# Kernel optimization log

Measured on AMD Instinct MI355X. Metric: run time of the kernel, lower is better.

## Reference

```python
import jax, jax.numpy as jnp
import numpy as np

N_NODES = 100000
N_EDGES = 1600000
HIDDEN = 64
EPS = 1e-5


def setup_inputs() -> dict:
    key = jax.random.key(0)
    ks = jax.random.split(key, 12)
    h = HIDDEN
    inp = {
        'x': jax.random.normal(ks[0], (N_NODES, h), dtype=jnp.float32),
        'edge_index': jax.random.randint(ks[1], (2, N_EDGES), 0, N_NODES, dtype=jnp.int32),
        'message': jax.random.normal(ks[2], (N_EDGES, h), dtype=jnp.float32),
        # node_mlp: Linear(2h->h), BN(h), ReLU, Dropout(identity), Linear(h->h), BN(h), ReLU
        'W1': jax.random.normal(ks[3], (2 * h, h), dtype=jnp.float32) / np.sqrt(2.0 * h),
        'b1': jnp.zeros((h,), jnp.float32),
        'g1': jnp.ones((h,), jnp.float32),
        'be1': jnp.zeros((h,), jnp.float32),
        'W2': jax.random.normal(ks[4], (h, h), dtype=jnp.float32) / np.sqrt(h),
        'b2': jnp.zeros((h,), jnp.float32),
        'g2': jnp.ones((h,), jnp.float32),
        'be2': jnp.zeros((h,), jnp.float32),
        # attention_mlp: Linear(h->1), Sigmoid
        'Wa': jax.random.normal(ks[5], (h, 1), dtype=jnp.float32) / np.sqrt(h),
        'ba': jnp.zeros((1,), jnp.float32),
    }
    return inp


def _scatter_max(msg, idx, n):
    # torch_scatter scatter(..., reduce='max') fills segments with no edges with 0
    agg = jax.ops.segment_max(msg, idx, num_segments=n)  # [N, H], -inf where empty
    cnt = jax.ops.segment_sum(jnp.ones((idx.shape[0],), msg.dtype), idx, num_segments=n)
    return jnp.where(cnt[:, None] > 0, agg, jnp.zeros((), msg.dtype))


def _batchnorm(x, gamma, beta):
    # training-mode BatchNorm1d: batch mean / biased variance
    mu = jnp.mean(x, axis=0)
    var = jnp.mean((x - mu) ** 2, axis=0)
    return (x - mu) * jax.lax.rsqrt(var + EPS) * gamma + beta


def reference(x, edge_index, message, W1, b1, g1, be1, W2, b2, g2, be2, Wa, ba):
    n = x.shape[0]
    row, col = edge_index[0], edge_index[1]
    fwd = _scatter_max(message, col, n)   # [N, H]
    bwd = _scatter_max(message, row, n)   # [N, H]
    out = jnp.concatenate([fwd, bwd], axis=1)          # [N, 2H]
    h1 = jax.nn.relu(_batchnorm(out @ W1 + b1, g1, be1))  # dropout = identity (eval)
    h2 = jax.nn.relu(_batchnorm(h1 @ W2 + b2, g2, be2))   # [N, H]
    att = jax.nn.sigmoid(h2 @ Wa + ba).reshape(-1)          # [N]
    return (h2, att)
```

## Files before the change

### kernel.cpp

```cpp
#include <hip/hip_runtime.h>
#include <hip/hip_bf16.h>
#include <cstdint>
#include <cstddef>

#define HDIM 64
#define EPS 1e-5f
#define BN 128
#define BSH 7
#define NXCD 8
#define BCAPX 2560
#define CURPAD 16
#define SENTE 128u
static const unsigned SENT = 0x007FFFFFu;

typedef short bf16x8 __attribute__((ext_vector_type(8)));
typedef float f32x4  __attribute__((ext_vector_type(4)));
typedef float f4v    __attribute__((ext_vector_type(4)));
typedef unsigned u2v __attribute__((ext_vector_type(2)));
typedef unsigned u4v __attribute__((ext_vector_type(4)));

__device__ __forceinline__ unsigned bf16rn(float f) {
    unsigned u = __float_as_uint(f);
    return (u + 0x7FFFu + ((u >> 16) & 1u)) >> 16;
}

__device__ __forceinline__ unsigned flipf(float f) {
    unsigned u = __float_as_uint(f);
    return u ^ (((unsigned)((int)u >> 31)) | 0x80000000u);
}

__device__ __forceinline__ float unflip(unsigned u) {
    if (u == SENT) return 0.0f;
    unsigned b = (u & 0x80000000u) ? (u & 0x7FFFFFFFu) : ~u;
    return __uint_as_float(b);
}

__global__ __launch_bounds__(256) void fill_kernel(
    const int* __restrict__ ei, unsigned* __restrict__ bcur,
    unsigned* __restrict__ entries,
    const float* __restrict__ W1, const float* __restrict__ W2,
    unsigned short* __restrict__ W1T, unsigned short* __restrict__ W2T,
    int E, int nblk, int eblocks) {
    int blk = blockIdx.x;
    if (blk >= eblocks) {
        int t = (blk - eblocks) * 256 + threadIdx.x;
        if (t < 128 * 64) {
            int k = t >> 6, o = t & 63;
            W1T[o * 128 + k] = (unsigned short)bf16rn(W1[t]);
        } else {
            int t2 = t - 128 * 64;
            if (t2 < 64 * 64) {
                int k = t2 >> 6, o = t2 & 63;
                W2T[o * 64 + k] = (unsigned short)bf16rn(W2[t2]);
            }
        }
        return;
    }
    int e = blk * 256 + threadIdx.x;
    if (e >= E) return;
    unsigned xcd;
    asm volatile("s_getreg_b32 %0, hwreg(HW_REG_XCC_ID)" : "=s"(xcd));
    xcd &= (NXCD - 1);
    int row = ei[e];
    int col = ei[(size_t)E + e];
    unsigned cell1 = (unsigned)(col >> BSH) * NXCD + xcd;
    unsigned cell2 = (unsigned)(nblk + (row >> BSH)) * NXCD + xcd;
    unsigned p1 = atomicAdd(&bcur[(size_t)cell1 * CURPAD], 1u);
    unsigned p2 = atomicAdd(&bcur[(size_t)cell2 * CURPAD], 1u);
    if (p1 < BCAPX)
        entries[(size_t)cell1 * BCAPX + p1] = ((unsigned)e << 8) | (unsigned)(col & (BN - 1));
    if (p2 < BCAPX)
        entries[(size_t)cell2 * BCAPX + p2] = ((unsigned)e << 8) | (unsigned)(row & (BN - 1));
}

__global__ __launch_bounds__(256) void binned_max_kernel(
    const float* __restrict__ msg, const unsigned* __restrict__ bcur,
    const unsigned* __restrict__ entries,
    unsigned short* __restrict__ fwdB, unsigned short* __restrict__ bwdB,
    int N, int nblk) {
    __shared__ __align__(16) unsigned acc[(BN + 1) * HDIM];
    int tid = threadIdx.x;
    int wave = tid >> 6, lane = tid & 63;
    int b = blockIdx.x;

    {
        u4v sv; sv.x = SENT; sv.y = SENT; sv.z = SENT; sv.w = SENT;
        u4v* p = (u4v*)acc;
        for (int i = tid; i < (BN + 1) * HDIM / 4; i += 256) p[i] = sv;
    }
    __syncthreads();

    unsigned accBase = (unsigned)(size_t)&acc[0];
    unsigned laneOff = accBase + ((unsigned)lane << 2);

    for (int rr = 0; rr < 2; ++rr) {
        int r = wave + rr * 4;
        unsigned cnt = bcur[((size_t)b * NXCD + r) * CURPAD];
        if (cnt > BCAPX) cnt = BCAPX;
        if (cnt == 0) continue;
        const unsigned* rb = entries + ((size_t)b * NXCD + r) * BCAPX;

        unsigned cur = ((unsigned)lane < cnt) ? rb[lane] : SENTE;
        float v[16];
#pragma unroll
        for (int k = 0; k < 16; ++k) {
            unsigned ent = __shfl(cur, k);
            v[k] = __builtin_nontemporal_load(&msg[(size_t)(ent >> 8) * HDIM + lane]);
        }

        for (unsigned c0 = 0; c0 < cnt; c0 += 64) {
            unsigned rem = cnt - c0;
            unsigned nxt = SENTE;
            bool havenxt = (c0 + 64 < cnt);
            if (havenxt)
                nxt = (c0 + 64 + (unsigned)lane < cnt) ? rb[c0 + 64 + lane] : SENTE;
#pragma unroll
            for (int b16 = 0; b16 < 4; ++b16) {
                if ((unsigned)(b16 * 16) >= rem) break;
                bool hn = (c0 + (unsigned)((b16 + 1) * 16) < cnt);
                float vn[16];
                if (hn) {
                    unsigned src = (b16 < 3) ? cur : nxt;
                    int kb = (b16 < 3) ? (b16 + 1) * 16 : 0;
#pragma unroll
                    for (int k = 0; k < 16; ++k) {
                        unsigned ent = __shfl(src, kb + k);
                        vn[k] = __builtin_nontemporal_load(
                            &msg[(size_t)(ent >> 8) * HDIM + lane]);
                    }
                }
#pragma unroll
                for (int k = 0; k < 16; ++k) {
                    unsigned ent = __shfl(cur, b16 * 16 + k);
                    unsigned addr = laneOff + ((ent & 255u) << 8);
                    asm volatile("ds_max_u32 %0, %1" :: "v"(addr), "v"(flipf(v[k])));
                }
                if (hn) {
#pragma unroll
                    for (int k = 0; k < 16; ++k) v[k] = vn[k];
                }
            }
            cur = nxt;
        }
    }
    asm volatile("" ::: "memory");
    __syncthreads();

    bool fwd = (b < nblk);
    int node0 = (fwd ? b : b - nblk) * BN;
    unsigned short* dst = fwd ? fwdB : bwdB;
    for (int i = tid; i < BN * (HDIM / 4); i += 256) {
        int rrow = i >> 4, c4 = (i & 15) * 4;
        int node = node0 + rrow;
        if (node >= N) continue;
        uint4 a = *(const uint4*)&acc[rrow * HDIM + c4];
        float v0 = unflip(a.x), v1 = unflip(a.y);
        float v2 = unflip(a.z), v3 = unflip(a.w);
        u2v o;
        o.x = bf16rn(v0) | (bf16rn(v1) << 16);
        o.y = bf16rn(v2) | (bf16rn(v3) << 16);
        *(u2v*)(dst + (size_t)node * HDIM + c4) = o;
    }
}


__global__ __launch_bounds__(256) void gemm1_mfma_kernel(
    const unsigned short* __restrict__ fwdB, const unsigned short* __restrict__ bwdB,
    const unsigned short* __restrict__ W1T, const float* __restrict__ b1,
    float* __restrict__ y1, float* __restrict__ sum1, float* __restrict__ sq1, int N) {
    __shared__ float wsum[4][64], wsq[4][64];
    int tid = threadIdx.x;
    int wave = tid >> 6, lane = tid & 63;
    int lrow = lane & 15, kseg = lane >> 4;
    int rbase = blockIdx.x * 64 + wave * 16;

    bf16x8 bfr[4][4];
#pragma unroll
    for (int nt = 0; nt < 4; ++nt)
#pragma unroll
        for (int kb = 0; kb < 4; ++kb)
            bfr[nt][kb] = *(const bf16x8*)(W1T + (size_t)(nt * 16 + lrow) * 128 + kb * 32 + kseg * 8);

    int r = rbase + lrow;
    bool ok = (r < N);
    size_t ro = (size_t)(ok ? r : 0) * HDIM;
    bf16x8 z = {};
    bf16x8 afr[4];
    afr[0] = *(const bf16x8*)(fwdB + ro + kseg * 8);
    afr[1] = *(const bf16x8*)(fwdB + ro + 32 + kseg * 8);
    afr[2] = *(const bf16x8*)(bwdB + ro + kseg * 8);
    afr[3] = *(const bf16x8*)(bwdB + ro + 32 + kseg * 8);
    if (!ok) { afr[0] = z; afr[1] = z; afr[2] = z; afr[3] = z; }

    f32x4 acc[4] = {};
#pragma unroll
    for (int kb = 0; kb < 4; ++kb)
#pragma unroll
        for (int nt = 0; nt < 4; ++nt)
            acc[nt] = __builtin_amdgcn_mfma_f32_16x16x32_bf16(afr[kb], bfr[nt][kb], acc[nt], 0, 0, 0);

#pragma unroll
    for (int nt = 0; nt < 4; ++nt) {
        int col = nt * 16 + lrow;
        float bias = b1[col];
        float s = 0.f, q = 0.f;
#pragma unroll
        for (int rr = 0; rr < 4; ++rr) {
            int rowi = rbase + kseg * 4 + rr;
            if (rowi < N) {
                float v = acc[nt][rr] + bias;
                y1[(size_t)rowi * HDIM + col] = v;
                s += v; q += v * v;
            }
        }
        s += __shfl_xor(s, 16); s += __shfl_xor(s, 32);
        q += __shfl_xor(q, 16); q += __shfl_xor(q, 32);
        if (kseg == 0) { wsum[wave][col] = s; wsq[wave][col] = q; }
    }
    __syncthreads();
    if (tid < 64) {
        float S = wsum[0][tid] + wsum[1][tid] + wsum[2][tid] + wsum[3][tid];
        float Q = wsq[0][tid] + wsq[1][tid] + wsq[2][tid] + wsq[3][tid];
        atomicAdd(&sum1[tid], S);
        atomicAdd(&sq1[tid], Q);
    }
}

__global__ __launch_bounds__(256) void gemm2_mfma_kernel(
    const float* __restrict__ y1, const float* __restrict__ sum1, const float* __restrict__ sq1,
    const float* __restrict__ g1, const float* __restrict__ be1,
    const unsigned short* __restrict__ W2T, const float* __restrict__ b2,
    float* __restrict__ y2, float* __restrict__ sum2, float* __restrict__ sq2, int N) {
    __shared__ float sc[64], sh[64];
    __shared__ float wsum[4][64], wsq[4][64];
    int tid = threadIdx.x;
    if (tid < 64) {
        float invN = 1.0f / (float)N;
        float mu = sum1[tid] * invN;
        float var = sq1[tid] * invN - mu * mu;
        float rs = rsqrtf(var + EPS);
        float s = rs * g1[tid];
        sc[tid] = s;
        sh[tid] = be1[tid] - mu * s;
    }
    __syncthreads();
    int wave = tid >> 6, lane = tid & 63;
    int lrow = lane & 15, kseg = lane >> 4;
    int rbase = blockIdx.x * 64 + wave * 16;

    bf16x8 bfr[4][2];
#pragma unroll
    for (int nt = 0; nt < 4; ++nt)
#pragma unroll
        for (int kb = 0; kb < 2; ++kb)
            bfr[nt][kb] = *(const bf16x8*)(W2T + (size_t)(nt * 16 + lrow) * 64 + kb * 32 + kseg * 8);

    int r = rbase + lrow;
    size_t ro = (size_t)((r < N) ? r : 0) * HDIM;
    bf16x8 afr[2];
#pragma unroll
    for (int kb = 0; kb < 2; ++kb) {
        const f4v* yp = (const f4v*)(y1 + ro + kb * 32 + kseg * 8);
        f4v u0 = yp[0], u1 = yp[1];
        int k0 = kb * 32 + kseg * 8;
        bf16x8 a;
#pragma unroll
        for (int j = 0; j < 4; ++j) {
            float h0 = fmaxf(fmaf(u0[j], sc[k0 + j], sh[k0 + j]), 0.f);
            float h1 = fmaxf(fmaf(u1[j], sc[k0 + 4 + j], sh[k0 + 4 + j]), 0.f);
            a[j] = (short)bf16rn(h0);
            a[4 + j] = (short)bf16rn(h1);
        }
        afr[kb] = a;
    }

    f32x4 acc[4] = {};
#pragma unroll
    for (int kb = 0; kb < 2; ++kb)
#pragma unroll
        for (int nt = 0; nt < 4; ++nt)
            acc[nt] = __builtin_amdgcn_mfma_f32_16x16x32_bf16(afr[kb], bfr[nt][kb], acc[nt], 0, 0, 0);

#pragma unroll
    for (int nt = 0; nt < 4; ++nt) {
        int col = nt * 16 + lrow;
        float bias = b2[col];
        float s = 0.f, q = 0.f;
#pragma unroll
        for (int rr = 0; rr < 4; ++rr) {
            int rowi = rbase + kseg * 4 + rr;
            if (rowi < N) {
                float v = acc[nt][rr] + bias;
                y2[(size_t)rowi * HDIM + col] = v;
                s += v; q += v * v;
            }
        }
        s += __shfl_xor(s, 16); s += __shfl_xor(s, 32);
        q += __shfl_xor(q, 16); q += __shfl_xor(q, 32);
        if (kseg == 0) { wsum[wave][col] = s; wsq[wave][col] = q; }
    }
    __syncthreads();
    if (tid < 64) {
        float S = wsum[0][tid] + wsum[1][tid] + wsum[2][tid] + wsum[3][tid];
        float Q = wsq[0][tid] + wsq[1][tid] + wsq[2][tid] + wsq[3][tid];
        atomicAdd(&sum2[tid], S);
        atomicAdd(&sq2[tid], Q);
    }
}

__global__ __launch_bounds__(256) void final_kernel(
    const float* __restrict__ y2, const float* __restrict__ sum2, const float* __restrict__ sq2,
    const float* __restrict__ g2, const float* __restrict__ be2,
    const float* __restrict__ Wa, const float* __restrict__ ba,
    float* __restrict__ out_h2, float* __restrict__ out_att, int N) {
    __shared__ float sc[HDIM], sh[HDIM], wa[HDIM];
    __shared__ float bav;
    if (threadIdx.x < HDIM) {
        int c = threadIdx.x;
        float invN = 1.0f / (float)N;
        float mu = sum2[c] * invN;
        float var = sq2[c] * invN - mu * mu;
        float rstd = rsqrtf(var + EPS);
        float s = rstd * g2[c];
        sc[c] = s;
        sh[c] = be2[c] - mu * s;
        wa[c] = Wa[c];
    }
    if (threadIdx.x == 0) bav = ba[0];
    __syncthreads();
    int n = blockIdx.x * 256 + threadIdx.x;
    if (n >= N) return;

    const f4v* p = (const f4v*)&y2[(size_t)n * HDIM];
    f4v* dst = (f4v*)&out_h2[(size_t)n * HDIM];
    float att = bav;
#pragma unroll 1
    for (int kk = 0; kk < 16; ++kk) {
        f4v u = p[kk];
        f4v hv;
#pragma unroll
        for (int j = 0; j < 4; ++j) {
            int k = kk * 4 + j;
            float h = fmaxf(fmaf(u[j], sc[k], sh[k]), 0.0f);
            hv[j] = h;
            att = fmaf(h, wa[k], att);
        }
        dst[kk] = hv;
    }
    out_att[n] = 1.0f / (1.0f + expf(-att));
}

extern "C" void kernel_launch(void* const* d_in, const int* in_sizes, int n_in,
                              void* d_out, int out_size, void* d_ws, size_t ws_size,
                              hipStream_t stream) {
    const int*   ei   = (const int*)d_in[1];
    const float* msg  = (const float*)d_in[2];
    const float* W1   = (const float*)d_in[3];
    const float* b1   = (const float*)d_in[4];
    const float* g1   = (const float*)d_in[5];
    const float* be1  = (const float*)d_in[6];
    const float* W2   = (const float*)d_in[7];
    const float* b2   = (const float*)d_in[8];
    const float* g2   = (const float*)d_in[9];
    const float* be2  = (const float*)d_in[10];
    const float* Wa   = (const float*)d_in[11];
    const float* ba   = (const float*)d_in[12];

    const int N = in_sizes[0] / HDIM;
    const int E = in_sizes[1] / 2;
    const int nblk = (N + BN - 1) / BN;

    unsigned short* fwdB = (unsigned short*)d_ws;
    unsigned short* bwdB = fwdB + (size_t)N * HDIM;
    unsigned short* W1T  = bwdB + (size_t)N * HDIM;
    unsigned short* W2T  = W1T + 8192;
    float*    stats      = (float*)(W2T + 4096);
    unsigned* bcur       = (unsigned*)(stats + 256);
    unsigned* entries    = bcur + (size_t)2 * nblk * NXCD * CURPAD;
    float*    y1         = (float*)d_out;
    float*    y2         = (float*)d_ws;
    float*    out_att    = (float*)d_out + (size_t)N * HDIM;

    hipMemsetAsync(stats, 0, 256 * sizeof(float)
                             + (size_t)2 * nblk * NXCD * CURPAD * sizeof(unsigned), stream);

    int eblocks = (E + 255) / 256;
    fill_kernel<<<eblocks + 48, 256, 0, stream>>>(ei, bcur, entries, W1, W2,
                                                  W1T, W2T, E, nblk, eblocks);

    binned_max_kernel<<<2 * nblk, 256, 0, stream>>>(msg, bcur, entries, fwdB, bwdB, N, nblk);

    int G = (N + 63) / 64;
    gemm1_mfma_kernel<<<G, 256, 0, stream>>>(fwdB, bwdB, W1T, b1, y1,
                                             stats, stats + 64, N);
    gemm2_mfma_kernel<<<G, 256, 0, stream>>>(y1, stats, stats + 64, g1, be1,
                                             W2T, b2, y2, stats + 128, stats + 192, N);
    final_kernel<<<(N + 255) / 256, 256, 0, stream>>>(y2, stats + 128, stats + 192,
                                                      g2, be2, Wa, ba,
                                                      (float*)d_out, out_att, N);
}
```

Measured before the change: 439.3 us.

## Use 16-byte vector message loads with padded LDS rows in binned max

Each lane in the binned max kernel now loads four contiguous floats with a 16-byte nontemporal load, so one wave instruction covers four edges at a time instead of one. To limit bank conflicts when four edges from the same wave hit different rows, the LDS accumulator rows are padded to a stride of 68 words. The old software prefetch of the next batch of messages is removed, which cuts register pressure but may expose more load latency.

Result: faster. 428.9 us, median of 2 (-2.4%).

```diff
diff --git a/kernel.cpp b/kernel.cpp
--- a/kernel.cpp
+++ b/kernel.cpp
@@ -11,6 +11,7 @@
 #define BCAPX 2560
 #define CURPAD 16
 #define SENTE 128u
+#define LSTRIDE 68
 static const unsigned SENT = 0x007FFFFFu;
 
 typedef short bf16x8 __attribute__((ext_vector_type(8)));
@@ -78,20 +79,21 @@
     const unsigned* __restrict__ entries,
     unsigned short* __restrict__ fwdB, unsigned short* __restrict__ bwdB,
     int N, int nblk) {
-    __shared__ __align__(16) unsigned acc[(BN + 1) * HDIM];
+    __shared__ __align__(16) unsigned acc[(BN + 1) * LSTRIDE];
     int tid = threadIdx.x;
     int wave = tid >> 6, lane = tid & 63;
+    int part = lane & 15, grp = lane >> 4;
     int b = blockIdx.x;
 
     {
         u4v sv; sv.x = SENT; sv.y = SENT; sv.z = SENT; sv.w = SENT;
         u4v* p = (u4v*)acc;
-        for (int i = tid; i < (BN + 1) * HDIM / 4; i += 256) p[i] = sv;
+        for (int i = tid; i < (BN + 1) * LSTRIDE / 4; i += 256) p[i] = sv;
     }
     __syncthreads();
 
     unsigned accBase = (unsigned)(size_t)&acc[0];
-    unsigned laneOff = accBase + ((unsigned)lane << 2);
+    unsigned partOff = accBase + ((unsigned)part << 4);
 
     for (int rr = 0; rr < 2; ++rr) {
         int r = wave + rr * 4;
@@ -100,47 +102,30 @@
         if (cnt == 0) continue;
         const unsigned* rb = entries + ((size_t)b * NXCD + r) * BCAPX;
 
-        unsigned cur = ((unsigned)lane < cnt) ? rb[lane] : SENTE;
-        float v[16];
-#pragma unroll
-        for (int k = 0; k < 16; ++k) {
-            unsigned ent = __shfl(cur, k);
-            v[k] = __builtin_nontemporal_load(&msg[(size_t)(ent >> 8) * HDIM + lane]);
-        }
-
         for (unsigned c0 = 0; c0 < cnt; c0 += 64) {
+            unsigned myent = (c0 + (unsigned)lane < cnt) ? rb[c0 + lane] : SENTE;
             unsigned rem = cnt - c0;
-            unsigned nxt = SENTE;
-            bool havenxt = (c0 + 64 < cnt);
-            if (havenxt)
-                nxt = (c0 + 64 + (unsigned)lane < cnt) ? rb[c0 + 64 + lane] : SENTE;
 #pragma unroll
             for (int b16 = 0; b16 < 4; ++b16) {
                 if ((unsigned)(b16 * 16) >= rem) break;
-                bool hn = (c0 + (unsigned)((b16 + 1) * 16) < cnt);
-                float vn[16];
-                if (hn) {
-                    unsigned src = (b16 < 3) ? cur : nxt;
-                    int kb = (b16 < 3) ? (b16 + 1) * 16 : 0;
-#pragma unroll
-                    for (int k = 0; k < 16; ++k) {
-                        unsigned ent = __shfl(src, kb + k);
-                        vn[k] = __builtin_nontemporal_load(
-                            &msg[(size_t)(ent >> 8) * HDIM + lane]);
-                    }
+                unsigned ents[4];
+                f4v m[4];
+#pragma unroll
+                for (int s = 0; s < 4; ++s) {
+                    ents[s] = __shfl(myent, b16 * 16 + s * 4 + grp);
+                    m[s] = __builtin_nontemporal_load(
+                        (const f4v*)&msg[(size_t)(ents[s] >> 8) * HDIM + part * 4]);
                 }
 #pragma unroll
-                for (int k = 0; k < 16; ++k) {
-                    unsigned ent = __shfl(cur, b16 * 16 + k);
-                    unsigned addr = laneOff + ((ent & 255u) << 8);
-                    asm volatile("ds_max_u32 %0, %1" :: "v"(addr), "v"(flipf(v[k])));
-                }
-                if (hn) {
-#pragma unroll
-                    for (int k = 0; k < 16; ++k) v[k] = vn[k];
+                for (int s = 0; s < 4; ++s) {
+                    unsigned loc = ents[s] & 255u;
+                    unsigned a0 = partOff + loc * (LSTRIDE * 4u);
+                    asm volatile("ds_max_u32 %0, %1" :: "v"(a0),      "v"(flipf(m[s].x)));
+                    asm volatile("ds_max_u32 %0, %1" :: "v"(a0 + 4u), "v"(flipf(m[s].y)));
+                    asm volatile("ds_max_u32 %0, %1" :: "v"(a0 + 8u), "v"(flipf(m[s].z)));
+                    asm volatile("ds_max_u32 %0, %1" :: "v"(a0 + 12u),"v"(flipf(m[s].w)));
                 }
             }
-            cur = nxt;
         }
     }
     asm volatile("" ::: "memory");
@@ -153,7 +138,7 @@
         int rrow = i >> 4, c4 = (i & 15) * 4;
         int node = node0 + rrow;
         if (node >= N) continue;
-        uint4 a = *(const uint4*)&acc[rrow * HDIM + c4];
+        uint4 a = *(const uint4*)&acc[rrow * LSTRIDE + c4];
         float v0 = unflip(a.x), v1 = unflip(a.y);
         float v2 = unflip(a.z), v3 = unflip(a.w);
         u2v o;
```
